# Kernel optimization log

Hardware: AMD Instinct MI355X
Metric: run time of the kernel (lower is better)

Reference implementation:

```python
import math
import jax, jax.numpy as jnp
import numpy as np

HEADS = 8


def setup_inputs() -> dict:
    key = jax.random.key(0)
    k1, k2, k3 = jax.random.split(key, 3)
    bs, C, H, Wd = 16, 512, 32, 32
    x = jax.random.normal(k1, (bs, C, H, Wd), dtype=jnp.float32)
    pos_enc = jax.random.normal(k2, (bs, C, H, Wd), dtype=jnp.float32)
    # 1x1 conv: weight [3C, C], bias [3C]
    W = jax.random.normal(k3, (3 * C, C), dtype=jnp.float32) * (1.0 / math.sqrt(C))
    b = jnp.zeros((3 * C,), dtype=jnp.float32)
    return {"x": x, "pos_enc": pos_enc, "W": W, "b": b}


def reference(x, pos_enc, W, b):
    x = x + pos_enc
    bs, C, H, Wd = x.shape
    heads = HEADS
    dim = C // heads
    N = H * Wd
    # 1x1 conv == channel matmul
    c = jnp.einsum('oc,bchw->bohw', W, x) + b[None, :, None, None]
    c = c.reshape(bs, 3, heads, dim, N)
    q = c[:, 0]  # [bs, heads, dim, N]
    k = c[:, 1]
    v = c[:, 2]
    scale = 1.0 / math.sqrt(dim)
    attn = jnp.einsum('bhdn,bhdm->bhnm', q, k) * scale  # [bs, heads, N, N]
    attn = jax.nn.softmax(attn, axis=-1)
    out = jnp.einsum('bhdm,bhnm->bhdn', v, attn)  # [bs, heads, dim, N]
    return x + out.reshape(bs, C, H, Wd)
```

## Files before the change

kernel.cpp:

```cpp
#include <hip/hip_runtime.h>
#include <stdint.h>


typedef __attribute__((ext_vector_type(4))) float f32x4;
typedef __attribute__((ext_vector_type(16))) float f32x16;
typedef __attribute__((ext_vector_type(8))) __bf16 bf16x8;
typedef __attribute__((ext_vector_type(8))) short short8;
typedef __attribute__((ext_vector_type(4))) short short4v;
typedef __attribute__((ext_vector_type(4))) int int4v;

#define DEVINL static __device__ __forceinline__

DEVINL unsigned short f2bf(float f) {
  unsigned u = __builtin_bit_cast(unsigned, f);
  u += 0x7FFFu + ((u >> 16) & 1u);
  return (unsigned short)(u >> 16);
}

DEVINL void gload16(const void* g, const void* lds) {
  __builtin_amdgcn_global_load_lds(
      (const __attribute__((address_space(1))) unsigned int*)(uintptr_t)g,
      (__attribute__((address_space(3))) unsigned int*)(uintptr_t)lds, 16, 0, 0);
}

DEVINL int cvtpk(float lo, float hi) {
  int d;
  asm("v_cvt_pk_bf16_f32 %0, %1, %2" : "=v"(d) : "v"(lo), "v"(hi));
  return d;
}

__global__ __launch_bounds__(256) void k_conv(const float* __restrict__ Wf,
                                              unsigned short* __restrict__ wbo) {
  const int i = (blockIdx.x * 256 + threadIdx.x) * 4;
  const f32x4 v = *(const f32x4*)(Wf + i);
  short4v t;
  t[0] = (short)f2bf(v[0]); t[1] = (short)f2bf(v[1]);
  t[2] = (short)f2bf(v[2]); t[3] = (short)f2bf(v[3]);
  *(short4v*)(wbo + i) = t;
}

__global__ __launch_bounds__(256) void k_addt(const float* __restrict__ x,
                                              const float* __restrict__ pe,
                                              float* __restrict__ out,
                                              unsigned short* __restrict__ st) {
  __shared__ unsigned short T[64][64];
  const int b = blockIdx.z, ct = blockIdx.y, nt = blockIdx.x;
  const int tid = threadIdx.x;
  const int cl = tid >> 4, n4 = (tid & 15) * 4;
  const size_t base = ((size_t)b * 512 + ct * 64) * 1024 + nt * 64;
#pragma unroll
  for (int i = 0; i < 4; ++i) {
    const int c = cl + i * 16;
    const size_t idx = base + (size_t)c * 1024 + n4;
    const f32x4 xv = *(const f32x4*)(x + idx);
    const f32x4 pv = *(const f32x4*)(pe + idx);
    const f32x4 s = xv + pv;
    *(f32x4*)(out + idx) = s;
    short4v t;
    t[0] = (short)f2bf(s[0]); t[1] = (short)f2bf(s[1]);
    t[2] = (short)f2bf(s[2]); t[3] = (short)f2bf(s[3]);
    *(short4v*)&T[c][n4] = t;
  }
  __syncthreads();
  const int nl = tid >> 2, cq = tid & 3;
  short8 v0, v1;
#pragma unroll
  for (int j = 0; j < 8; ++j) {
    v0[j] = (short)T[cq * 16 + j][nl];
    v1[j] = (short)T[cq * 16 + 8 + j][nl];
  }
  const size_t so = ((size_t)b * 1024 + nt * 64 + nl) * 512 + ct * 64 + cq * 16;
  *(short8*)(st + so) = v0;
  *(short8*)(st + so + 8) = v1;
}

__global__ __launch_bounds__(256, 2) void k_gemm(const unsigned short* __restrict__ st,
                                                 const unsigned short* __restrict__ wb,
                                                 const float* __restrict__ bias,
                                                 unsigned short* __restrict__ qb,
                                                 unsigned short* __restrict__ kb,
                                                 unsigned short* __restrict__ vb) {
  const int b = blockIdx.z;
  const int mode = (blockIdx.y >= 8);
  const int tile_m = (mode ? (blockIdx.y - 8) : blockIdx.y) * 128;
  const int tile_n = blockIdx.x * 128;
  const unsigned short* Ag;
  const unsigned short* Bg;
  if (!mode) {
    Ag = st + (size_t)b * 524288 + (size_t)tile_m * 512;
    Bg = wb + (size_t)tile_n * 512;
  } else {
    Ag = wb + (size_t)(1024 + tile_m) * 512;
    Bg = st + (size_t)b * 524288 + (size_t)tile_n * 512;
  }
  __shared__ unsigned short As[4096];
  __shared__ unsigned short Bs[4096];
  const int tid = threadIdx.x, lane = tid & 63, w = tid >> 6;
  const int wrow = w >> 1, wcol = w & 1, lr = lane & 15, g = lane >> 4;
  f32x4 acc[4][4] = {};
  for (int kt = 0; kt < 16; ++kt) {
    __syncthreads();
#pragma unroll
    for (int j = 0; j < 2; ++j) {
      const int D = j * 4096 + w * 1024 + lane * 16;
      const int row = D >> 6, off = D & 63;
      gload16((const char*)Ag + (size_t)row * 1024 + kt * 64 + off,
              (const char*)As + j * 4096 + w * 1024);
      gload16((const char*)Bg + (size_t)row * 1024 + kt * 64 + off,
              (const char*)Bs + j * 4096 + w * 1024);
    }
    __syncthreads();
    bf16x8 a[4], bb[4];
#pragma unroll
    for (int i = 0; i < 4; ++i) {
      a[i]  = *(const bf16x8*)(As + (wrow * 64 + i * 16 + lr) * 32 + g * 8);
      bb[i] = *(const bf16x8*)(Bs + (wcol * 64 + i * 16 + lr) * 32 + g * 8);
    }
#pragma unroll
    for (int i = 0; i < 4; ++i)
#pragma unroll
      for (int jj = 0; jj < 4; ++jj)
        acc[i][jj] = __builtin_amdgcn_mfma_f32_16x16x32_bf16(a[i], bb[jj], acc[i][jj], 0, 0, 0);
  }
  if (!mode) {
#pragma unroll
    for (int jj = 0; jj < 4; ++jj) {
      const int o = tile_n + wcol * 64 + jj * 16 + lr;
      const float bv = bias[o];
      unsigned short* dst = (o < 512) ? qb : kb;
      const size_t rowbase = ((size_t)b * 8 + ((o >> 6) & 7)) * 1024;
      const int d = o & 63;
#pragma unroll
      for (int i = 0; i < 4; ++i) {
        const int n0 = tile_m + wrow * 64 + i * 16 + g * 4;
#pragma unroll
        for (int r = 0; r < 4; ++r)
          dst[(rowbase + n0 + r) * 64 + d] = f2bf(acc[i][jj][r] + bv);
      }
    }
  } else {
#pragma unroll
    for (int i = 0; i < 4; ++i) {
#pragma unroll
      for (int r = 0; r < 4; ++r) {
        const int oh = tile_m + wrow * 64 + i * 16 + g * 4 + r;
        const float bv = bias[1024 + oh];
        const size_t rb = (((size_t)b * 8 + (oh >> 6)) * 64 + (oh & 63)) * 1024;
#pragma unroll
        for (int jj = 0; jj < 4; ++jj) {
          const int n = tile_n + wcol * 64 + jj * 16 + lr;
          vb[rb + n] = f2bf(acc[i][jj][r] + bv);
        }
      }
    }
  }
}

__global__ __launch_bounds__(256, 4) void k_attn(const unsigned short* __restrict__ qb,
                                                 const unsigned short* __restrict__ kb,
                                                 const unsigned short* __restrict__ vb,
                                                 float* __restrict__ out) {
  __shared__ __align__(16) char smem[32768];

  const int f = blockIdx.x;
  const int bh = (f & 7) * 16 + ((f >> 3) & 15);
  const int qt = f >> 7;

  const int tid = threadIdx.x, lane = tid & 63, w = tid >> 6;
  const int ln = lane & 31, hf = lane >> 5;
  const float F = 0.18033688011112042f;

  const char* kbase = (const char*)kb + (size_t)bh * 131072;
  const char* vbase = (const char*)vb + (size_t)bh * 131072;

  const char* qrow = (const char*)qb + ((size_t)bh * 1024 + qt * 128 + w * 32 + ln) * 128;
  bf16x8 qf[4];
#pragma unroll
  for (int c = 0; c < 4; ++c) qf[c] = *(const bf16x8*)(qrow + c * 32 + hf * 16);

  f32x16 O0 = {}, O1 = {};
  float mF = -__builtin_inff(), lsum = 0.f;

#define STAGE(mt_, buf_)                                                          \
  {                                                                               \
    char* Kd = smem + (buf_) * 8192 + w * 1024;                                   \
    char* Vd = smem + 16384 + (buf_) * 8192 + w * 1024;                           \
    _Pragma("unroll") for (int j = 0; j < 2; ++j) {                               \
      const int D = j * 4096 + w * 1024 + lane * 16;                              \
      const int row = D >> 7, ch = (D >> 4) & 7;                                  \
      const int sw = (ch ^ (row & 7)) * 16;                                       \
      gload16(kbase + (size_t)((mt_) * 64 + row) * 128 + sw, Kd + j * 4096);      \
      gload16(vbase + (size_t)row * 2048 + (mt_) * 128 + sw, Vd + j * 4096);      \
    }                                                                             \
  }

  STAGE(0, 0);
  __syncthreads();
  int buf = 0;
  for (int mt = 0; mt < 16; ++mt) {
    if (mt < 15) STAGE(mt + 1, buf ^ 1);
    const char* Kc = smem + buf * 8192;
    const char* Vc = smem + 16384 + buf * 8192;

    f32x16 s0 = {}, s1 = {};
#pragma unroll
    for (int c = 0; c < 4; ++c) {
      const int cb = ((c * 2 + hf) ^ (ln & 7)) * 16;
      const bf16x8 k0 = *(const bf16x8*)(Kc + ln * 128 + cb);
      s0 = __builtin_amdgcn_mfma_f32_32x32x16_bf16(k0, qf[c], s0, 0, 0, 0);
      const bf16x8 k1 = *(const bf16x8*)(Kc + (32 + ln) * 128 + cb);
      s1 = __builtin_amdgcn_mfma_f32_32x32x16_bf16(k1, qf[c], s1, 0, 0, 0);
    }

    float t = fmaxf(s0[0], s1[0]);
#pragma unroll
    for (int r = 1; r < 16; ++r) t = fmaxf(t, fmaxf(s0[r], s1[r]));
    t = fmaxf(t, __shfl_xor(t, 32));
    const float tF = t * F;
    if (!__all(tF <= mF + 8.f)) {
      const float mN = fmaxf(mF, tF);
      const float al = __builtin_amdgcn_exp2f(mF - mN);
#pragma unroll
      for (int r = 0; r < 16; ++r) { O0[r] *= al; O1[r] *= al; }
      lsum *= al;
      mF = mN;
    }

#pragma unroll
    for (int r = 0; r < 16; ++r) s0[r] = __builtin_amdgcn_exp2f(fmaf(s0[r], F, -mF));
#pragma unroll
    for (int r = 0; r < 16; ++r) s1[r] = __builtin_amdgcn_exp2f(fmaf(s1[r], F, -mF));

    {
      const f32x16 ps = s0 + s1;
      float a0 = (ps[0] + ps[1]) + (ps[2] + ps[3]);
      float a1 = (ps[4] + ps[5]) + (ps[6] + ps[7]);
      float a2 = (ps[8] + ps[9]) + (ps[10] + ps[11]);
      float a3 = (ps[12] + ps[13]) + (ps[14] + ps[15]);
      float sm = (a0 + a1) + (a2 + a3);
      lsum += sm + __shfl_xor(sm, 32);
    }

    int c0[8], c1[8];
#pragma unroll
    for (int j = 0; j < 8; ++j) {
      c0[j] = cvtpk(s0[2 * j], s0[2 * j + 1]);
      c1[j] = cvtpk(s1[2 * j], s1[2 * j + 1]);
    }
    int pw[4][4];
#pragma unroll
    for (int half = 0; half < 2; ++half) {
      const int* cc = half ? c1 : c0;
#pragma unroll
      for (int q = 0; q < 2; ++q) {
        const int b4 = q * 4, ch = half * 2 + q;
        const int p0 = __shfl_xor(cc[b4 + 0], 32);
        const int p1 = __shfl_xor(cc[b4 + 1], 32);
        const int p2 = __shfl_xor(cc[b4 + 2], 32);
        const int p3 = __shfl_xor(cc[b4 + 3], 32);
        pw[ch][0] = hf ? p2 : cc[b4 + 0];
        pw[ch][1] = hf ? p3 : cc[b4 + 1];
        pw[ch][2] = hf ? cc[b4 + 2] : p0;
        pw[ch][3] = hf ? cc[b4 + 3] : p1;
      }
    }

#pragma unroll
    for (int c = 0; c < 4; ++c) {
      const int4v t4 = {pw[c][0], pw[c][1], pw[c][2], pw[c][3]};
      const bf16x8 pb = __builtin_bit_cast(bf16x8, t4);
      const int cb = ((c * 2 + hf) ^ (ln & 7)) * 16;
      const bf16x8 v0 = *(const bf16x8*)(Vc + ln * 128 + cb);
      O0 = __builtin_amdgcn_mfma_f32_32x32x16_bf16(v0, pb, O0, 0, 0, 0);
      const bf16x8 v1 = *(const bf16x8*)(Vc + (32 + ln) * 128 + cb);
      O1 = __builtin_amdgcn_mfma_f32_32x32x16_bf16(v1, pb, O1, 0, 0, 0);
    }

    __syncthreads();
    buf ^= 1;
  }
#undef STAGE

  const float inv = 1.0f / lsum;
  float* obase = out + ((size_t)bh * 64) * 1024 + qt * 128 + w * 32 + ln;
#pragma unroll
  for (int r = 0; r < 16; ++r) {
    const int d0 = (r & 3) + 8 * (r >> 2) + 4 * hf;
    obase[(size_t)d0 * 1024] += O0[r] * inv;
    obase[(size_t)(d0 + 32) * 1024] += O1[r] * inv;
  }
}

extern "C" void kernel_launch(void* const* d_in, const int* in_sizes, int n_in,
                              void* d_out, int out_size, void* d_ws, size_t ws_size,
                              hipStream_t stream) {
  const float* x    = (const float*)d_in[0];
  const float* pe   = (const float*)d_in[1];
  const float* W    = (const float*)d_in[2];
  const float* bias = (const float*)d_in[3];
  float* out = (float*)d_out;
  char* ws = (char*)d_ws;
  unsigned short* wb = (unsigned short*)(ws);
  unsigned short* st = (unsigned short*)(ws + ((size_t)2 << 20));
  unsigned short* qb = (unsigned short*)(ws + ((size_t)18 << 20));
  unsigned short* kb = (unsigned short*)(ws + ((size_t)34 << 20));
  unsigned short* vb = (unsigned short*)(ws + ((size_t)50 << 20));

  k_conv<<<dim3(768), dim3(256), 0, stream>>>(W, wb);
  k_addt<<<dim3(16, 8, 16), dim3(256), 0, stream>>>(x, pe, out, st);
  k_gemm<<<dim3(8, 12, 16), dim3(256), 0, stream>>>(st, wb, bias, qb, kb, vb);
  k_attn<<<dim3(1024), dim3(256), 0, stream>>>(qb, kb, vb, out);
}
```

Measured before the change: 215.1 us.

## Remap GEMM blocks per XCD, raise occupancy, use permlane32 swap in attention

The QKV GEMM moves to a 1D grid whose block index is remapped so each XCD handles a contiguous range of batch/tile work, which should improve L2 locality. Its launch bounds also rise from 2 to 4 waves per SIMD, which may limit registers and cause spills. In the attention kernel, the cross-half P exchange is done with v_permlane32_swap instead of four shuffles plus selects per group, cutting cross-lane traffic in the PV loop.

```diff
diff --git a/kernel.cpp b/kernel.cpp
--- a/kernel.cpp
+++ b/kernel.cpp
@@ -27,6 +27,10 @@
   int d;
   asm("v_cvt_pk_bf16_f32 %0, %1, %2" : "=v"(d) : "v"(lo), "v"(hi));
   return d;
+}
+
+DEVINL void pl32swap(int& a, int& b) {
+  asm("v_permlane32_swap_b32 %0, %1" : "+v"(a), "+v"(b));
 }
 
 __global__ __launch_bounds__(256) void k_conv(const float* __restrict__ Wf,
@@ -74,16 +78,21 @@
   *(short8*)(st + so + 8) = v1;
 }
 
-__global__ __launch_bounds__(256, 2) void k_gemm(const unsigned short* __restrict__ st,
+__global__ __launch_bounds__(256, 4) void k_gemm(const unsigned short* __restrict__ st,
                                                  const unsigned short* __restrict__ wb,
                                                  const float* __restrict__ bias,
                                                  unsigned short* __restrict__ qb,
                                                  unsigned short* __restrict__ kb,
                                                  unsigned short* __restrict__ vb) {
-  const int b = blockIdx.z;
-  const int mode = (blockIdx.y >= 8);
-  const int tile_m = (mode ? (blockIdx.y - 8) : blockIdx.y) * 128;
-  const int tile_n = blockIdx.x * 128;
+  const int fid = blockIdx.x;
+  const int xcd = fid & 7, s = fid >> 3;
+  const int t = xcd * 24 + (s >> 3);
+  const int bx = s & 7;
+  const int by = t % 12;
+  const int b = t / 12;
+  const int mode = (by >= 8);
+  const int tile_m = (mode ? (by - 8) : by) * 128;
+  const int tile_n = bx * 128;
   const unsigned short* Ag;
   const unsigned short* Bg;
   if (!mode) {
@@ -250,18 +259,14 @@
     int pw[4][4];
 #pragma unroll
     for (int half = 0; half < 2; ++half) {
-      const int* cc = half ? c1 : c0;
+      int* cc = half ? c1 : c0;
 #pragma unroll
       for (int q = 0; q < 2; ++q) {
         const int b4 = q * 4, ch = half * 2 + q;
-        const int p0 = __shfl_xor(cc[b4 + 0], 32);
-        const int p1 = __shfl_xor(cc[b4 + 1], 32);
-        const int p2 = __shfl_xor(cc[b4 + 2], 32);
-        const int p3 = __shfl_xor(cc[b4 + 3], 32);
-        pw[ch][0] = hf ? p2 : cc[b4 + 0];
-        pw[ch][1] = hf ? p3 : cc[b4 + 1];
-        pw[ch][2] = hf ? cc[b4 + 2] : p0;
-        pw[ch][3] = hf ? cc[b4 + 3] : p1;
+        pl32swap(cc[b4 + 0], cc[b4 + 2]);
+        pl32swap(cc[b4 + 1], cc[b4 + 3]);
+        pw[ch][0] = cc[b4 + 0]; pw[ch][1] = cc[b4 + 1];
+        pw[ch][2] = cc[b4 + 2]; pw[ch][3] = cc[b4 + 3];
       }
     }
 
@@ -308,6 +313,6 @@
 
   k_conv<<<dim3(768), dim3(256), 0, stream>>>(W, wb);
   k_addt<<<dim3(16, 8, 16), dim3(256), 0, stream>>>(x, pe, out, st);
-  k_gemm<<<dim3(8, 12, 16), dim3(256), 0, stream>>>(st, wb, bias, qb, kb, vb);
+  k_gemm<<<dim3(1536), dim3(256), 0, stream>>>(st, wb, bias, qb, kb, vb);
   k_attn<<<dim3(1024), dim3(256), 0, stream>>>(qb, kb, vb, out);
 }
```

Result: faster. 209.6 us (-2.5%).
